# Kernel tuning notes

Measured on AMD Instinct MI355X. Metric: run time of the kernel, lower is better.

Reference implementation:

```python
import jax, jax.numpy as jnp
import numpy as np

NUM_HEADS = 8
NUM_LEVELS = 4
NUM_POINTS = 4
EMBED = 256
HEAD_DIM = EMBED // NUM_HEADS
SPATIAL = [(100, 100), (50, 50), (25, 25), (13, 13)]  # (H, W) per level


def _bilinear_sample(val, grid):
    """torch.nn.functional.grid_sample(mode='bilinear', padding_mode='zeros', align_corners=False).
    val: [B, H, W, C], grid: [B, N, 2] with (x, y) in [-1, 1]. Returns [B, N, C]."""
    B, H, W, C = val.shape
    x = (grid[..., 0] + 1.0) * (W * 0.5) - 0.5
    y = (grid[..., 1] + 1.0) * (H * 0.5) - 0.5
    x0 = jnp.floor(x)
    y0 = jnp.floor(y)
    wx1 = x - x0
    wy1 = y - y0
    wx0 = 1.0 - wx1
    wy0 = 1.0 - wy1
    x0i = x0.astype(jnp.int32)
    y0i = y0.astype(jnp.int32)
    valf = val.reshape(B, H * W, C)

    def corner(xi, yi, w):
        valid = (xi >= 0) & (xi < W) & (yi >= 0) & (yi < H)
        idx = jnp.clip(yi, 0, H - 1) * W + jnp.clip(xi, 0, W - 1)
        v = jnp.take_along_axis(valf, idx[..., None], axis=1)  # [B, N, C]
        return v * (w * valid)[..., None]

    return (corner(x0i, y0i, wx0 * wy0) + corner(x0i + 1, y0i, wx1 * wy0)
            + corner(x0i, y0i + 1, wx0 * wy1) + corner(x0i + 1, y0i + 1, wx1 * wy1))


def setup_inputs() -> dict:
    key = jax.random.key(0)
    ks = jax.random.split(key, 12)
    bs, nq = 4, 6000
    nv = sum(h * w for h, w in SPATIAL)
    s = 0.02
    return {
        "query": jax.random.normal(ks[0], (bs, nq, EMBED), jnp.float32),
        "value": jax.random.normal(ks[1], (bs, nv, EMBED), jnp.float32),
        "reference_points": jax.random.uniform(ks[2], (bs, nq, NUM_LEVELS, 2), jnp.float32),
        "W_off": jax.random.normal(ks[3], (EMBED, NUM_HEADS * NUM_LEVELS * NUM_POINTS * 2), jnp.float32) * s,
        "b_off": jax.random.normal(ks[4], (NUM_HEADS * NUM_LEVELS * NUM_POINTS * 2,), jnp.float32),
        "W_attn": jax.random.normal(ks[5], (EMBED, NUM_HEADS * NUM_LEVELS * NUM_POINTS), jnp.float32) * s,
        "b_attn": jnp.zeros((NUM_HEADS * NUM_LEVELS * NUM_POINTS,), jnp.float32),
        "W_val": jax.random.normal(ks[6], (EMBED, EMBED), jnp.float32) * s,
        "b_val": jnp.zeros((EMBED,), jnp.float32),
        "W_out": jax.random.normal(ks[7], (EMBED, EMBED), jnp.float32) * s,
        "b_out": jnp.zeros((EMBED,), jnp.float32),
        "spatial_shapes": jnp.asarray(np.array(SPATIAL, dtype=np.int32)),
    }


def reference(query, value, reference_points, W_off, b_off, W_attn, b_attn,
              W_val, b_val, W_out, b_out, spatial_shapes):
    shapes = [(int(h), int(w)) for h, w in np.asarray(spatial_shapes)]
    bs, nq, _ = query.shape
    nv = value.shape[1]

    v = (value @ W_val + b_val).reshape(bs, nv, NUM_HEADS, HEAD_DIM)
    offsets = (query @ W_off + b_off).reshape(bs, nq, NUM_HEADS, NUM_LEVELS, NUM_POINTS, 2)
    aw = (query @ W_attn + b_attn).reshape(bs, nq, NUM_HEADS, NUM_LEVELS * NUM_POINTS)
    aw = jax.nn.softmax(aw, axis=-1).reshape(bs, nq, NUM_HEADS, NUM_LEVELS, NUM_POINTS)

    # offset normalizer is [W, H] per level
    norm = jnp.asarray([[w, h] for h, w in shapes], dtype=query.dtype)  # [L, 2]
    loc = reference_points[:, :, None, :, None, :] + offsets / norm[None, None, None, :, None, :]
    grids = 2.0 * loc - 1.0  # [bs, nq, H, L, P, 2]
    # -> [bs*H, nq*P, 2] per level
    grids = jnp.transpose(grids, (0, 2, 1, 3, 4, 5)).reshape(bs * NUM_HEADS, nq, NUM_LEVELS, NUM_POINTS, 2)

    v_bh = jnp.transpose(v, (0, 2, 1, 3)).reshape(bs * NUM_HEADS, nv, HEAD_DIM)
    sampled = []
    start = 0
    for l, (H_, W_) in enumerate(shapes):
        val_l = v_bh[:, start:start + H_ * W_].reshape(bs * NUM_HEADS, H_, W_, HEAD_DIM)
        grid_l = grids[:, :, l].reshape(bs * NUM_HEADS, nq * NUM_POINTS, 2)
        s_l = _bilinear_sample(val_l, grid_l).reshape(bs * NUM_HEADS, nq, NUM_POINTS, HEAD_DIM)
        sampled.append(s_l)
        start += H_ * W_
    sampled = jnp.stack(sampled, axis=2)  # [bs*H, nq, L, P, c]

    aw_bh = jnp.transpose(aw, (0, 2, 1, 3, 4)).reshape(bs * NUM_HEADS, nq, NUM_LEVELS, NUM_POINTS)
    out = (sampled * aw_bh[..., None]).sum(axis=(2, 3))  # [bs*H, nq, c]
    out = out.reshape(bs, NUM_HEADS, nq, HEAD_DIM).transpose(0, 2, 1, 3).reshape(bs, nq, EMBED)
    out = out @ W_out + b_out
    return out + query
```

## Files before the change

### kernel.cpp

```cpp
#include <hip/hip_runtime.h>
#include <hip/hip_bf16.h>

#define BS 4
#define NQ 6000
#define NV 13294
#define NH 8
#define HD 32
#define EMB 256
#define MV (BS * NV)
#define MQ (BS * NQ)

typedef __attribute__((ext_vector_type(8))) short short8;
typedef __attribute__((ext_vector_type(4))) float floatx4;

__device__ __constant__ float LVL_DIM[4] = {100.f, 50.f, 25.f, 13.f};

__device__ inline unsigned short bf16bits(float f) {
  __hip_bfloat16 h = __float2bfloat16(f);
  return *reinterpret_cast<unsigned short*>(&h);
}
__device__ inline unsigned int pk2bf(float lo, float hi) {
  return (unsigned int)bf16bits(lo) | ((unsigned int)bf16bits(hi) << 16);
}
__device__ inline float bflo(unsigned int u) { return __uint_as_float(u << 16); }
__device__ inline float bfhi(unsigned int u) { return __uint_as_float(u & 0xffff0000u); }

#define LDSTR 40
#define TILEU (128 * LDSTR)

__global__ __launch_bounds__(256) void wtrans_kernel(
    const float* __restrict__ W_val, const float* __restrict__ W_off,
    const float* __restrict__ W_attn, const float* __restrict__ W_out,
    unsigned short* __restrict__ Wt_val, unsigned short* __restrict__ Wt_qcat,
    unsigned short* __restrict__ Wt_out) {
  __shared__ float tile[32][33];
  const int b = blockIdx.x;
  const int x = threadIdx.x & 31, ty = threadIdx.x >> 5;

  const float* src;
  unsigned short* dst;
  int k0, n0;
  if (b < 64) {
    src = W_val;
    dst = Wt_val;
    k0 = (b >> 3) * 32;
    n0 = (b & 7) * 32;
  } else if (b < 128) {
    const int bb = b - 64;
    src = W_off;
    dst = Wt_qcat;
    k0 = (bb >> 3) * 32;
    n0 = (bb & 7) * 32;
  } else if (b < 160) {
    const int bb = b - 128;
    src = W_attn;
    dst = Wt_qcat + 256 * EMB;
    k0 = (bb >> 2) * 32;
    n0 = (bb & 3) * 32;
#pragma unroll
    for (int i = 0; i < 4; ++i)
      tile[ty + 8 * i][x] = src[(size_t)(k0 + ty + 8 * i) * 128 + n0 + x];
    __syncthreads();
#pragma unroll
    for (int i = 0; i < 4; ++i)
      dst[(size_t)(n0 + ty + 8 * i) * EMB + k0 + x] =
          bf16bits(tile[x][ty + 8 * i]);
    return;
  } else {
    const int bb = b - 160;
    src = W_out;
    dst = Wt_out;
    k0 = (bb >> 3) * 32;
    n0 = (bb & 7) * 32;
  }
#pragma unroll
  for (int i = 0; i < 4; ++i)
    tile[ty + 8 * i][x] = src[(size_t)(k0 + ty + 8 * i) * 256 + n0 + x];
  __syncthreads();
#pragma unroll
  for (int i = 0; i < 4; ++i)
    dst[(size_t)(n0 + ty + 8 * i) * EMB + k0 + x] = bf16bits(tile[x][ty + 8 * i]);
}

__device__ inline void loadA32(const float* __restrict__ A, int M, int m0,
                               int k0, int tid, float4 ra[4]) {
  const int r = tid >> 1, kh = (tid & 1) * 16;
  const int row = m0 + r;
  if (row < M) {
    const float* src = A + (size_t)row * EMB + k0 + kh;
#pragma unroll
    for (int j = 0; j < 4; ++j) ra[j] = *(const float4*)(src + 4 * j);
  } else {
#pragma unroll
    for (int j = 0; j < 4; ++j) ra[j] = make_float4(0.f, 0.f, 0.f, 0.f);
  }
}
__device__ inline void storeA32(unsigned short* lds, int tid,
                                const float4 ra[4]) {
  const int r = tid >> 1, kh = (tid & 1) * 16;
  unsigned short* dst = lds + r * LDSTR + kh;
  uint4 u0, u1;
  u0.x = pk2bf(ra[0].x, ra[0].y);
  u0.y = pk2bf(ra[0].z, ra[0].w);
  u0.z = pk2bf(ra[1].x, ra[1].y);
  u0.w = pk2bf(ra[1].z, ra[1].w);
  u1.x = pk2bf(ra[2].x, ra[2].y);
  u1.y = pk2bf(ra[2].z, ra[2].w);
  u1.z = pk2bf(ra[3].x, ra[3].y);
  u1.w = pk2bf(ra[3].z, ra[3].w);
  *(uint4*)(dst) = u0;
  *(uint4*)(dst + 8) = u1;
}
__device__ inline void loadBb(const unsigned short* __restrict__ B, int NB,
                              int n0, int k0, int tid, uint4 rb[2]) {
  const int r = tid >> 1, kh = (tid & 1) * 16;
  const int row = n0 + r;
  if (row < NB) {
    const unsigned short* src = B + (size_t)row * EMB + k0 + kh;
    rb[0] = *(const uint4*)(src);
    rb[1] = *(const uint4*)(src + 8);
  } else {
    rb[0] = make_uint4(0, 0, 0, 0);
    rb[1] = make_uint4(0, 0, 0, 0);
  }
}
__device__ inline void storeBb(unsigned short* lds, int tid,
                               const uint4 rb[2]) {
  const int r = tid >> 1, kh = (tid & 1) * 16;
  unsigned short* dst = lds + r * LDSTR + kh;
  *(uint4*)(dst) = rb[0];
  *(uint4*)(dst + 8) = rb[1];
}

__device__ inline void mfma_step32(const unsigned short* ldsA,
                                   const unsigned short* ldsB, int wm, int wn,
                                   int lane, floatx4 acc[4][4]) {
  const unsigned short* ap =
      ldsA + (wm * 64 + (lane & 15)) * LDSTR + (lane >> 4) * 8;
  const unsigned short* bp =
      ldsB + (wn * 64 + (lane & 15)) * LDSTR + (lane >> 4) * 8;
  short8 af[4], bfr[4];
#pragma unroll
  for (int t = 0; t < 4; ++t) {
    af[t] = *(const short8*)(ap + t * 16 * LDSTR);
    bfr[t] = *(const short8*)(bp + t * 16 * LDSTR);
  }
#pragma unroll
  for (int mt = 0; mt < 4; ++mt)
#pragma unroll
    for (int nt = 0; nt < 4; ++nt)
      acc[mt][nt] = __builtin_amdgcn_mfma_f32_16x16x32_bf16(af[mt], bfr[nt],
                                                            acc[mt][nt], 0, 0, 0);
}

__device__ inline void gemm_loop32_f32A(const float* __restrict__ A, int M,
                                        int m0,
                                        const unsigned short* __restrict__ B,
                                        int NB, int n0, unsigned short* lds,
                                        int tid, int wm, int wn, int lane,
                                        floatx4 acc[4][4]) {
  unsigned short* bufA[2] = {lds, lds + 2 * TILEU};
  unsigned short* bufB[2] = {lds + TILEU, lds + 3 * TILEU};
  float4 sa[2][4];
  uint4 sb[2][2];
  loadA32(A, M, m0, 0, tid, sa[0]);
  loadBb(B, NB, n0, 0, tid, sb[0]);
  loadA32(A, M, m0, 32, tid, sa[1]);
  loadBb(B, NB, n0, 32, tid, sb[1]);
  storeA32(bufA[0], tid, sa[0]);
  storeBb(bufB[0], tid, sb[0]);
  __syncthreads();
#pragma unroll
  for (int k = 0; k < 8; ++k) {
    const int cur = k & 1, nxt = cur ^ 1;
    if (k + 2 < 8) {
      loadA32(A, M, m0, (k + 2) * 32, tid, sa[k & 1]);
      loadBb(B, NB, n0, (k + 2) * 32, tid, sb[k & 1]);
    }
    if (k + 1 < 8) {
      storeA32(bufA[nxt], tid, sa[(k + 1) & 1]);
      storeBb(bufB[nxt], tid, sb[(k + 1) & 1]);
    }
    mfma_step32(bufA[cur], bufB[cur], wm, wn, lane, acc);
    __syncthreads();
  }
}

__device__ inline void gemm_loop32_bf16A(const unsigned short* __restrict__ A,
                                         int M, int m0,
                                         const unsigned short* __restrict__ B,
                                         int NB, int n0, unsigned short* lds,
                                         int tid, int wm, int wn, int lane,
                                         floatx4 acc[4][4]) {
  unsigned short* bufA[2] = {lds, lds + 2 * TILEU};
  unsigned short* bufB[2] = {lds + TILEU, lds + 3 * TILEU};
  uint4 sa[2][2], sb[2][2];
  loadBb(A, M, m0, 0, tid, sa[0]);
  loadBb(B, NB, n0, 0, tid, sb[0]);
  loadBb(A, M, m0, 32, tid, sa[1]);
  loadBb(B, NB, n0, 32, tid, sb[1]);
  storeBb(bufA[0], tid, sa[0]);
  storeBb(bufB[0], tid, sb[0]);
  __syncthreads();
#pragma unroll
  for (int k = 0; k < 8; ++k) {
    const int cur = k & 1, nxt = cur ^ 1;
    if (k + 2 < 8) {
      loadBb(A, M, m0, (k + 2) * 32, tid, sa[k & 1]);
      loadBb(B, NB, n0, (k + 2) * 32, tid, sb[k & 1]);
    }
    if (k + 1 < 8) {
      storeBb(bufA[nxt], tid, sa[(k + 1) & 1]);
      storeBb(bufB[nxt], tid, sb[(k + 1) & 1]);
    }
    mfma_step32(bufA[cur], bufB[cur], wm, wn, lane, acc);
    __syncthreads();
  }
}

__global__ __launch_bounds__(256, 2) void vproj_kernel(
    const float* __restrict__ value, const unsigned short* __restrict__ Wt_val,
    const float* __restrict__ b_val, unsigned short* __restrict__ vbh) {
  __shared__ unsigned short lds[4 * TILEU];
  const int tid = threadIdx.x, lane = tid & 63, w = tid >> 6;
  const int wm = w >> 1, wn = w & 1;
  floatx4 acc[4][4];
  const floatx4 zero = {0.f, 0.f, 0.f, 0.f};
#pragma unroll
  for (int i2 = 0; i2 < 4; i2++)
#pragma unroll
    for (int j = 0; j < 4; j++) acc[i2][j] = zero;
  const int quad = lane >> 4, cl = lane & 15;

  const int chunk = blockIdx.x >> 4, i = blockIdx.x & 15;
  const int m0 = (chunk * 8 + (i & 7)) * 128;
  const int n0 = (i >> 3) * 128;
  gemm_loop32_f32A(value, MV, m0, Wt_val, 256, n0, lds, tid, wm, wn, lane,
                   acc);
#pragma unroll
  for (int mt = 0; mt < 4; ++mt) {
#pragma unroll
    for (int r = 0; r < 4; ++r) {
      const int row = m0 + wm * 64 + mt * 16 + quad * 4 + r;
      if (row < MV) {
        const int b = row / NV, n = row - b * NV;
#pragma unroll
        for (int nt = 0; nt < 4; ++nt) {
          const int c = n0 + wn * 64 + nt * 16 + cl;
          const int h = c >> 5, d = c & 31;
          vbh[(((size_t)(b * NH + h)) * NV + n) * HD + d] =
              bf16bits(acc[mt][nt][r] + b_val[c]);
        }
      }
    }
  }
}

__global__ __launch_bounds__(256, 2) void qproj_kernel(
    const float* __restrict__ query, const unsigned short* __restrict__ Wt_qcat,
    const float* __restrict__ refpts, const float* __restrict__ b_off,
    const float* __restrict__ b_attn, float* __restrict__ locbuf,
    float* __restrict__ awbuf) {
  __shared__ unsigned short lds[4 * TILEU];
  const int tid = threadIdx.x, lane = tid & 63, w = tid >> 6;
  const int wm = w >> 1, wn = w & 1;
  floatx4 acc[4][4];
  const floatx4 zero = {0.f, 0.f, 0.f, 0.f};
#pragma unroll
  for (int i2 = 0; i2 < 4; i2++)
#pragma unroll
    for (int j = 0; j < 4; j++) acc[i2][j] = zero;
  const int quad = lane >> 4, cl = lane & 15;

  const int bid = blockIdx.x;
  const int chunk = bid / 24, i = bid % 24;
  const int m_idx = chunk * 8 + (i & 7);
  if (m_idx >= 188) return;
  const int m0 = m_idx * 128;
  const int n0 = (i >> 3) * 128;
  gemm_loop32_f32A(query, MQ, m0, Wt_qcat, 384, n0, lds, tid, wm, wn, lane,
                   acc);
  if (n0 < 256) {
#pragma unroll
    for (int mt = 0; mt < 4; ++mt) {
#pragma unroll
      for (int r = 0; r < 4; ++r) {
        const int row = m0 + wm * 64 + mt * 16 + quad * 4 + r;
        if (row < MQ) {
#pragma unroll
          for (int nt = 0; nt < 4; ++nt) {
            const int c = n0 + wn * 64 + nt * 16 + cl;
            const int xy = c & 1, l = (c >> 3) & 3;
            const float dim = LVL_DIM[l];
            const float ref = refpts[(size_t)row * 8 + l * 2 + xy];
            locbuf[(size_t)row * 256 + c] =
                ref * dim + acc[mt][nt][r] + b_off[c] - 0.5f;
          }
        }
      }
    }
  } else {
#pragma unroll
    for (int mt = 0; mt < 4; ++mt) {
#pragma unroll
      for (int r = 0; r < 4; ++r) {
        const int row = m0 + wm * 64 + mt * 16 + quad * 4 + r;
        if (row < MQ) {
#pragma unroll
          for (int nt = 0; nt < 4; ++nt) {
            const int ca = wn * 64 + nt * 16 + cl;
            awbuf[(size_t)row * 128 + ca] = acc[mt][nt][r] + b_attn[ca];
          }
        }
      }
    }
  }
}

__global__ __launch_bounds__(256, 4) void sample_kernel(
    const unsigned short* __restrict__ vbh, const float* __restrict__ locbuf,
    const float* __restrict__ awbuf, unsigned short* __restrict__ sampledb) {
  const int blk = blockIdx.x;
  const int t = blk >> 3;
  const int quarter = t / 375;
  const int j = t - quarter * 375;
  const int slice = (blk & 7) * 4 + quarter;
  const int h = slice & 7;
  const int w = threadIdx.x >> 6;
  const int lane = threadIdx.x & 63;
  const int r0 = (slice >> 3) * NQ + j * 16 + w * 4;
  const int g = lane >> 2;
  const int d8 = lane & 3;
  const int l = g >> 2;

  const int W_ = (l < 2) ? ((l == 0) ? 100 : 50) : ((l == 2) ? 25 : 13);
  const int START = (l < 2) ? ((l == 0) ? 0 : 10000) : ((l == 2) ? 12500 : 13125);
  const unsigned int* base =
      (const unsigned int*)vbh + ((size_t)slice * NV + START) * 16 + d8 * 4;

  float acc[4][8];
#pragma unroll
  for (int rr = 0; rr < 4; ++rr) {
    const int row = r0 + rr;
    const float2 xy =
        *(const float2*)(locbuf + (size_t)row * 256 + h * 32 + g * 2);
    const float wl = awbuf[(size_t)row * 128 + h * 16 + g];
    float mx = wl;
    mx = fmaxf(mx, __shfl_xor(mx, 4));
    mx = fmaxf(mx, __shfl_xor(mx, 8));
    mx = fmaxf(mx, __shfl_xor(mx, 16));
    mx = fmaxf(mx, __shfl_xor(mx, 32));
    const float e = __expf(wl - mx);
    float ssum = e;
    ssum += __shfl_xor(ssum, 4);
    ssum += __shfl_xor(ssum, 8);
    ssum += __shfl_xor(ssum, 16);
    ssum += __shfl_xor(ssum, 32);
    const float wgt = e / ssum;

    const float fx = floorf(xy.x), fy = floorf(xy.y);
    const int x0 = (int)fx, y0 = (int)fy;
    const float wx1 = xy.x - fx, wy1 = xy.y - fy;
    const float wx0 = 1.f - wx1, wy0 = 1.f - wy1;
    const int x0c = min(max(x0, 0), W_ - 1), x1c = min(max(x0 + 1, 0), W_ - 1);
    const int y0c = min(max(y0, 0), W_ - 1), y1c = min(max(y0 + 1, 0), W_ - 1);
    const float mx0 = ((unsigned)x0 < (unsigned)W_) ? wx0 : 0.f;
    const float mx1 = ((unsigned)(x0 + 1) < (unsigned)W_) ? wx1 : 0.f;
    const float my0 = ((unsigned)y0 < (unsigned)W_) ? wy0 : 0.f;
    const float my1 = ((unsigned)(y0 + 1) < (unsigned)W_) ? wy1 : 0.f;
    const float wy0w = wgt * my0, wy1w = wgt * my1;
    const float w00 = wy0w * mx0, w01 = wy0w * mx1;
    const float w10 = wy1w * mx0, w11 = wy1w * mx1;

    const int rb0 = y0c * W_, rb1 = y1c * W_;
    const uint4 u00 = *(const uint4*)(base + (size_t)(rb0 + x0c) * 16);
    const uint4 u01 = *(const uint4*)(base + (size_t)(rb0 + x1c) * 16);
    const uint4 u10 = *(const uint4*)(base + (size_t)(rb1 + x0c) * 16);
    const uint4 u11 = *(const uint4*)(base + (size_t)(rb1 + x1c) * 16);
    const unsigned int* p00 = &u00.x;
    const unsigned int* p01 = &u01.x;
    const unsigned int* p10 = &u10.x;
    const unsigned int* p11 = &u11.x;
#pragma unroll
    for (int k = 0; k < 4; ++k) {
      acc[rr][2 * k] = w00 * bflo(p00[k]) + w01 * bflo(p01[k]) +
                       w10 * bflo(p10[k]) + w11 * bflo(p11[k]);
      acc[rr][2 * k + 1] = w00 * bfhi(p00[k]) + w01 * bfhi(p01[k]) +
                           w10 * bfhi(p10[k]) + w11 * bfhi(p11[k]);
    }
  }

  const bool b0 = (lane >> 2) & 1;
  const bool b1 = (lane >> 3) & 1;
  const bool b2 = (lane >> 4) & 1;
#pragma unroll
  for (int rr = 0; rr < 4; ++rr) {
    float* v = acc[rr];
#pragma unroll
    for (int jj = 0; jj < 4; ++jj) {
      float lo = v[jj], hi = v[jj + 4];
      float recv = __shfl_xor(b0 ? lo : hi, 4);
      v[jj] = (b0 ? hi : lo) + recv;
    }
#pragma unroll
    for (int jj = 0; jj < 2; ++jj) {
      float lo = v[jj], hi = v[jj + 2];
      float recv = __shfl_xor(b1 ? lo : hi, 8);
      v[jj] = (b1 ? hi : lo) + recv;
    }
    {
      float lo = v[0], hi = v[1];
      float recv = __shfl_xor(b2 ? lo : hi, 16);
      v[0] = (b2 ? hi : lo) + recv;
    }
    v[0] += __shfl_xor(v[0], 32);
  }

  const int dim = d8 * 8 + (b0 ? 4 : 0) + (b1 ? 2 : 0) + (b2 ? 1 : 0);
  const bool hi = (lane >= 32);
  const float v0 = hi ? acc[1][0] : acc[0][0];
  const float v1 = hi ? acc[3][0] : acc[2][0];
  const int row0 = r0 + (hi ? 1 : 0);
  const int row1 = r0 + 2 + (hi ? 1 : 0);
  sampledb[(size_t)row0 * EMB + h * 32 + dim] = bf16bits(v0);
  sampledb[(size_t)row1 * EMB + h * 32 + dim] = bf16bits(v1);
}

__global__ __launch_bounds__(256, 2) void oproj_kernel(
    const unsigned short* __restrict__ sampledb,
    const unsigned short* __restrict__ Wt, const float* __restrict__ b_out,
    const float* __restrict__ query, float* __restrict__ out) {
  __shared__ unsigned short lds[4 * TILEU];
  const int tid = threadIdx.x, lane = tid & 63, w = tid >> 6;
  const int wm = w >> 1, wn = w & 1;
  const int chunk = blockIdx.x >> 4, i = blockIdx.x & 15;
  const int m_idx = chunk * 8 + (i & 7);
  if (m_idx >= 188) return;
  const int m0 = m_idx * 128;
  const int n0 = (i >> 3) * 128;
  floatx4 acc[4][4];
  const floatx4 zero = {0.f, 0.f, 0.f, 0.f};
#pragma unroll
  for (int i2 = 0; i2 < 4; i2++)
#pragma unroll
    for (int j = 0; j < 4; j++) acc[i2][j] = zero;

  gemm_loop32_bf16A(sampledb, MQ, m0, Wt, 256, n0, lds, tid, wm, wn, lane,
                    acc);

  const int quad = lane >> 4, cl = lane & 15;
#pragma unroll
  for (int mt = 0; mt < 4; ++mt) {
#pragma unroll
    for (int r = 0; r < 4; ++r) {
      const int row = m0 + wm * 64 + mt * 16 + quad * 4 + r;
      if (row < MQ) {
#pragma unroll
        for (int nt = 0; nt < 4; ++nt) {
          const int c = n0 + wn * 64 + nt * 16 + cl;
          out[(size_t)row * EMB + c] =
              acc[mt][nt][r] + b_out[c] + query[(size_t)row * EMB + c];
        }
      }
    }
  }
}

extern "C" void kernel_launch(void* const* d_in, const int* in_sizes, int n_in,
                              void* d_out, int out_size, void* d_ws,
                              size_t ws_size, hipStream_t stream) {
  const float* query  = (const float*)d_in[0];
  const float* value  = (const float*)d_in[1];
  const float* refpts = (const float*)d_in[2];
  const float* W_off  = (const float*)d_in[3];
  const float* b_off  = (const float*)d_in[4];
  const float* W_attn = (const float*)d_in[5];
  const float* b_attn = (const float*)d_in[6];
  const float* W_val  = (const float*)d_in[7];
  const float* b_val  = (const float*)d_in[8];
  const float* W_out  = (const float*)d_in[9];
  const float* b_out  = (const float*)d_in[10];
  float* out = (float*)d_out;

  char* ws = (char*)d_ws;
  unsigned short* vbh = (unsigned short*)ws;
  float* locbuf = (float*)(ws + 27226112);
  float* awbuf = (float*)(ws + 51802112);
  unsigned short* sampledb = (unsigned short*)(ws + 64090112);
  unsigned short* Wt_val = (unsigned short*)(ws + 76378112);
  unsigned short* Wt_qcat = (unsigned short*)(ws + 76509184);
  unsigned short* Wt_out = (unsigned short*)(ws + 76705792);

  wtrans_kernel<<<224, 256, 0, stream>>>(W_val, W_off, W_attn, W_out, Wt_val,
                                         Wt_qcat, Wt_out);
  vproj_kernel<<<832, 256, 0, stream>>>(value, Wt_val, b_val, vbh);
  qproj_kernel<<<576, 256, 0, stream>>>(query, Wt_qcat, refpts, b_off, b_attn,
                                        locbuf, awbuf);
  sample_kernel<<<12000, 256, 0, stream>>>(vbh, locbuf, awbuf, sampledb);
  oproj_kernel<<<384, 256, 0, stream>>>(sampledb, Wt_out, b_out, query, out);
}
```

Baseline: 231.8 us.

## Use LDS-only barriers in GEMM loops and fuse softmax into projection epilogue

Replaces __syncthreads in the double-buffered GEMM loops with an inline-asm barrier that waits only on LDS counters, so in-flight global prefetch loads are not drained at each barrier. Separately, the attention-weight softmax moves from the sampling kernel into the query projection epilogue, using 16-lane shuffles across each head's columns, so sampling reads final weights directly. The custom barrier depends on the compiler not needing a vmcnt wait there, and the epilogue softmax adds shuffle work to the GEMM.

```diff
diff --git a/kernel.cpp b/kernel.cpp
--- a/kernel.cpp
+++ b/kernel.cpp
@@ -24,6 +24,10 @@
 }
 __device__ inline float bflo(unsigned int u) { return __uint_as_float(u << 16); }
 __device__ inline float bfhi(unsigned int u) { return __uint_as_float(u & 0xffff0000u); }
+
+__device__ inline void barrier_nodrain() {
+  asm volatile("s_waitcnt lgkmcnt(0)\n\ts_barrier" ::: "memory");
+}
 
 #define LDSTR 40
 #define TILEU (128 * LDSTR)
@@ -169,7 +173,7 @@
   loadBb(B, NB, n0, 32, tid, sb[1]);
   storeA32(bufA[0], tid, sa[0]);
   storeBb(bufB[0], tid, sb[0]);
-  __syncthreads();
+  barrier_nodrain();
 #pragma unroll
   for (int k = 0; k < 8; ++k) {
     const int cur = k & 1, nxt = cur ^ 1;
@@ -182,7 +186,7 @@
       storeBb(bufB[nxt], tid, sb[(k + 1) & 1]);
     }
     mfma_step32(bufA[cur], bufB[cur], wm, wn, lane, acc);
-    __syncthreads();
+    barrier_nodrain();
   }
 }
 
@@ -201,7 +205,7 @@
   loadBb(B, NB, n0, 32, tid, sb[1]);
   storeBb(bufA[0], tid, sa[0]);
   storeBb(bufB[0], tid, sb[0]);
-  __syncthreads();
+  barrier_nodrain();
 #pragma unroll
   for (int k = 0; k < 8; ++k) {
     const int cur = k & 1, nxt = cur ^ 1;
@@ -214,7 +218,7 @@
       storeBb(bufB[nxt], tid, sb[(k + 1) & 1]);
     }
     mfma_step32(bufA[cur], bufB[cur], wm, wn, lane, acc);
-    __syncthreads();
+    barrier_nodrain();
   }
 }
 
@@ -309,7 +313,19 @@
 #pragma unroll
           for (int nt = 0; nt < 4; ++nt) {
             const int ca = wn * 64 + nt * 16 + cl;
-            awbuf[(size_t)row * 128 + ca] = acc[mt][nt][r] + b_attn[ca];
+            float v = acc[mt][nt][r] + b_attn[ca];
+            float m = v;
+            m = fmaxf(m, __shfl_xor(m, 1));
+            m = fmaxf(m, __shfl_xor(m, 2));
+            m = fmaxf(m, __shfl_xor(m, 4));
+            m = fmaxf(m, __shfl_xor(m, 8));
+            float e = __expf(v - m);
+            float s = e;
+            s += __shfl_xor(s, 1);
+            s += __shfl_xor(s, 2);
+            s += __shfl_xor(s, 4);
+            s += __shfl_xor(s, 8);
+            awbuf[(size_t)row * 128 + ca] = e / s;
           }
         }
       }
@@ -344,19 +360,7 @@
     const int row = r0 + rr;
     const float2 xy =
         *(const float2*)(locbuf + (size_t)row * 256 + h * 32 + g * 2);
-    const float wl = awbuf[(size_t)row * 128 + h * 16 + g];
-    float mx = wl;
-    mx = fmaxf(mx, __shfl_xor(mx, 4));
-    mx = fmaxf(mx, __shfl_xor(mx, 8));
-    mx = fmaxf(mx, __shfl_xor(mx, 16));
-    mx = fmaxf(mx, __shfl_xor(mx, 32));
-    const float e = __expf(wl - mx);
-    float ssum = e;
-    ssum += __shfl_xor(ssum, 4);
-    ssum += __shfl_xor(ssum, 8);
-    ssum += __shfl_xor(ssum, 16);
-    ssum += __shfl_xor(ssum, 32);
-    const float wgt = e / ssum;
+    const float wgt = awbuf[(size_t)row * 128 + h * 16 + g];
 
     const float fx = floorf(xy.x), fy = floorf(xy.y);
     const int x0 = (int)fx, y0 = (int)fy;
```

New measurement: 240.1 us. 1.04x slower.
